# Kernel optimization log

Hardware: AMD Instinct MI355X
Metric: run time of the kernel (lower is better)

## Reference

```python
import jax, jax.numpy as jnp
import numpy as np

B, TMAX, C, H, NCLS = 256, 512, 128, 256, 400


def _lengths():
    rs = np.random.RandomState(0)
    lens = rs.randint(128, TMAX + 1, size=B)
    lens[0] = TMAX  # pin max length so T = TMAX
    return lens


def setup_inputs() -> dict:
    lens = _lengths()
    total = int(lens.sum())
    key = jax.random.key(0)
    ks = jax.random.split(key, 12)
    s_in, s_h = 1.0 / np.sqrt(C), 1.0 / np.sqrt(H)
    return {
        "input_features": jax.random.normal(ks[0], (total, C), jnp.float32),
        "segment_lengths": jnp.asarray(lens, jnp.int32),
        "W_ih": jax.random.normal(ks[1], (4 * H, C), jnp.float32) * s_h,
        "W_hh": jax.random.normal(ks[2], (4 * H, H), jnp.float32) * s_h,
        "b_ih": jax.random.normal(ks[3], (4 * H,), jnp.float32) * s_h,
        "b_hh": jax.random.normal(ks[4], (4 * H,), jnp.float32) * s_h,
        "h0_W1": jax.random.normal(ks[5], (C, C), jnp.float32) * s_in,
        "h0_W2": jax.random.normal(ks[6], (H, C), jnp.float32) * s_in,
        "c0_W1": jax.random.normal(ks[7], (C, C), jnp.float32) * s_in,
        "c0_W2": jax.random.normal(ks[8], (H, C), jnp.float32) * s_in,
        "fc_W": jax.random.normal(ks[9], (NCLS, H), jnp.float32) * s_h,
        "fc_b": jax.random.normal(ks[10], (NCLS,), jnp.float32) * s_h,
    }


def _lstm_step(x, h, c, W_ih, W_hh, b_ih, b_hh):
    # torch.nn.LSTMCell gate order: i, f, g, o
    gates = x @ W_ih.T + b_ih + h @ W_hh.T + b_hh
    i, f, g, o = jnp.split(gates, 4, axis=-1)
    c_new = jax.nn.sigmoid(f) * c + jax.nn.sigmoid(i) * jnp.tanh(g)
    h_new = jax.nn.sigmoid(o) * jnp.tanh(c_new)
    return h_new, c_new


def reference(input_features, segment_lengths, W_ih, W_hh, b_ih, b_hh,
              h0_W1, h0_W2, c0_W1, c0_W2, fc_W, fc_b):
    lens = np.asarray(segment_lengths)            # static ragged structure
    nb = lens.shape[0]
    T = int(lens.max())
    seg_id = np.repeat(np.arange(nb), lens)       # [total]
    offs = np.concatenate([np.arange(l) for l in lens])
    dt = input_features.dtype

    # pad_sequence(batch_first=True): [B, T, C]
    padded = jnp.zeros((nb, T, input_features.shape[1]), dt)
    padded = padded.at[jnp.asarray(seg_id), jnp.asarray(offs)].set(input_features)

    # 'input_means' in the original is actually a per-segment SUM
    sums = jax.ops.segment_sum(input_features, jnp.asarray(seg_id), num_segments=nb)
    h0 = jax.nn.relu(sums @ h0_W1.T) @ h0_W2.T
    c0 = jax.nn.relu(sums @ c0_W1.T) @ c0_W2.T

    def step(carry, x_t):
        h, c = carry
        h, c = _lstm_step(x_t, h, c, W_ih, W_hh, b_ih, b_hh)
        return (h, c), h

    xs = jnp.transpose(padded, (1, 0, 2))         # [T, B, C]
    _, h_outs = jax.lax.scan(step, (h0, c0), xs)  # [T, B, H]

    # Faithful to the original: h_outs is stacked time-first, yet indexed
    # h_outs[i, :segment_len] with i = batch index -> for segment i, mean over
    # the first min(len_i, B) BATCH rows of the hidden state at time t=i.
    lens_j = jnp.asarray(lens)
    mask = (jnp.arange(nb)[None, :] < lens_j[:, None]).astype(dt)   # [B(i), B(b)]
    count = jnp.minimum(lens_j, nb).astype(dt)                       # slice clamps at B
    fc_in = jnp.einsum('ib,ibh->ih', mask, h_outs[:nb]) / count[:, None]

    return fc_in @ fc_W.T + fc_b
```

## Files before the change

### kernel.cpp

```cpp
#include <hip/hip_runtime.h>
#include <hip/hip_bf16.h>
#include <stdint.h>

#define NB    256
#define CIN   128
#define HID   256
#define TST   256
#define NCLS  400

#define GRPS  16
#define MEMB  4
#define BPG   16
#define HPB   64
#define RPB   256
#define HXS   392
#define SPP   17

#define WS_SUMS   0u
#define WS_HEX    131072u
#define WS_C0     655360u
#define WS_TAGS   917504u
#define WS_PP     1048576u

typedef __attribute__((ext_vector_type(8))) short bf16x8;
typedef __attribute__((ext_vector_type(4))) float f32x4;
typedef unsigned long long u64;

__device__ __forceinline__ short f2bf(float f) {
  __hip_bfloat16 h = __float2bfloat16(f);
  return *reinterpret_cast<short*>(&h);
}
__device__ __forceinline__ float sigm(float v) { return 1.0f / (1.0f + __expf(-v)); }
__device__ __forceinline__ float tanh_(float v) {
  v = fminf(fmaxf(v, -15.0f), 15.0f);
  const float e = __expf(2.0f * v);
  return (e - 1.0f) / (e + 1.0f);
}

__global__ void k_segsum(const float* __restrict__ x, const int* __restrict__ lens,
                         float* __restrict__ sums) {
  const int b = blockIdx.x, t = threadIdx.x;
  __shared__ int   s_l[NB];
  __shared__ int   s_red[256];
  __shared__ float s_f[CIN];
  s_l[t] = lens[t];
  __syncthreads();
  int part = 0;
  for (int i = t; i < b; i += 256) part += s_l[i];
  s_red[t] = part; __syncthreads();
  for (int k = 128; k > 0; k >>= 1) { if (t < k) s_red[t] += s_red[t + k]; __syncthreads(); }
  const int off = s_red[0];
  const int len = s_l[b];
  const int c = t & 127, half = t >> 7;
  float a = 0.f;
  for (int r = half; r < len; r += 2) a += x[(size_t)(off + r) * CIN + c];
  if (half) s_f[c] = a;
  __syncthreads();
  if (!half) sums[b * CIN + c] = a + s_f[c];
}

__global__ void k_init(const float* __restrict__ sums,
                       const float* __restrict__ w1h, const float* __restrict__ w2h,
                       const float* __restrict__ w1c, const float* __restrict__ w2c,
                       u64* __restrict__ hexch, float* __restrict__ c0) {
  const int b = blockIdx.x, t = threadIdx.x;
  __shared__ float s_in[CIN], s_h[CIN], s_c[CIN];
  __shared__ __align__(8) short s_hb[HID];
  if (t < CIN) s_in[t] = sums[b * CIN + t];
  __syncthreads();
  {
    const int j = t & 127;
    const float* w = (t < CIN ? w1h : w1c) + j * CIN;
    float a = 0.f;
    #pragma unroll 8
    for (int k = 0; k < CIN; k++) a += s_in[k] * w[k];
    a = fmaxf(a, 0.f);
    if (t < CIN) s_h[j] = a; else s_c[j] = a;
  }
  __syncthreads();
  float ah = 0.f, ac = 0.f;
  const float* wh = w2h + t * CIN;
  const float* wc = w2c + t * CIN;
  #pragma unroll 8
  for (int k = 0; k < CIN; k++) { ah += s_h[k] * wh[k]; ac += s_c[k] * wc[k]; }
  s_hb[t] = f2bf(ah);
  c0[b * HID + t] = ac;
  __syncthreads();
  if (t < HID / 4)
    hexch[(size_t)b * 64 + t] = *(const u64*)&s_hb[t * 4];
}

__launch_bounds__(1024, 1)
__global__ void k_lstm(const float* __restrict__ x, const int* __restrict__ lens,
                       const float* __restrict__ Wih, const float* __restrict__ Whh,
                       const float* __restrict__ bih, const float* __restrict__ bhh,
                       const float* __restrict__ c0,
                       u64* __restrict__ hexch, float* __restrict__ pp,
                       int* __restrict__ tags) {
  const int p    = blockIdx.x;
  const int m    = p >> 4;
  const int grp  = p & 15;
  const int bat0 = grp * BPG;
  const int hid0 = m * HPB;

  const int t   = threadIdx.x;
  const int w   = t >> 6;
  const int kq  = w & 3;
  const int mq  = w >> 2;
  const int l15 = t & 15;
  const int hi  = (t >> 4) & 3;

  const int j2 = t & 63, b2 = t >> 6;
  const int ch = t & 127, bp2 = (t >> 7) * 2;

  __shared__ __align__(16) short s_hxb[BPG * HXS];
  __shared__ float s_part[4 * RPB * SPP];
  __shared__ float s_red[1024];
  __shared__ __align__(8) short s_hvalb[1024];
  __shared__ int   s_lens[NB];
  __shared__ int   s_off[BPG], s_len[BPG];

  if (t < NB) s_lens[t] = lens[t];
  __syncthreads();
  if (t < BPG) {
    int off = 0;
    for (int k = 0; k < bat0 + t; k++) off += s_lens[k];
    s_off[t] = off;
    s_len[t] = s_lens[bat0 + t];
  }
  __syncthreads();

  #define LOADA(AV, MT, KC) do {                                                   \
    const int lr_   = (MT) * 16 + l15;                                             \
    const int grow_ = (lr_ >> 6) * HID + hid0 + (lr_ & 63);                        \
    const int k0_   = kq * 96 + (KC) * 32 + hi * 8;                                \
    const float* src_ = (k0_ < CIN) ? (Wih + (size_t)grow_ * CIN + k0_)            \
                                    : (Whh + (size_t)grow_ * HID + (k0_ - CIN));   \
    const float4 f0_ = *(const float4*)(src_);                                     \
    const float4 f1_ = *(const float4*)(src_ + 4);                                 \
    AV[0]=f2bf(f0_.x); AV[1]=f2bf(f0_.y); AV[2]=f2bf(f0_.z); AV[3]=f2bf(f0_.w);    \
    AV[4]=f2bf(f1_.x); AV[5]=f2bf(f1_.y); AV[6]=f2bf(f1_.z); AV[7]=f2bf(f1_.w);    \
  } while (0)
  bf16x8 a00, a01, a02, a10, a11, a12, a20, a21, a22, a30, a31, a32;
  LOADA(a00, mq*4+0, 0); LOADA(a01, mq*4+0, 1); LOADA(a02, mq*4+0, 2);
  LOADA(a10, mq*4+1, 0); LOADA(a11, mq*4+1, 1); LOADA(a12, mq*4+1, 2);
  LOADA(a20, mq*4+2, 0); LOADA(a21, mq*4+2, 1); LOADA(a22, mq*4+2, 2);
  LOADA(a30, mq*4+3, 0); LOADA(a31, mq*4+3, 1); LOADA(a32, mq*4+3, 2);

  const float bias0 = bih[0*HID + hid0 + j2] + bhh[0*HID + hid0 + j2];
  const float bias1 = bih[1*HID + hid0 + j2] + bhh[1*HID + hid0 + j2];
  const float bias2 = bih[2*HID + hid0 + j2] + bhh[2*HID + hid0 + j2];
  const float bias3 = bih[3*HID + hid0 + j2] + bhh[3*HID + hid0 + j2];

  float c_reg = c0[(size_t)(bat0 + b2) * HID + hid0 + j2];

  float xp0, xp1;
  #define PREFX(S) do { \
    xp0 = ((S) < s_len[bp2+0]) ? x[(size_t)(s_off[bp2+0]+(S))*CIN+ch] : 0.f; \
    xp1 = ((S) < s_len[bp2+1]) ? x[(size_t)(s_off[bp2+1]+(S))*CIN+ch] : 0.f; \
  } while (0)
  #define STAGE(S) do { \
    s_hxb[(bp2+0)*HXS+ch] = f2bf(xp0); \
    s_hxb[(bp2+1)*HXS+ch] = f2bf(xp1); \
    const int b_ = t >> 6, q64_ = t & 63; \
    const int mem_ = q64_ >> 4; \
    if (mem_ == m && (S) > 0) { \
      *(u64*)&s_hxb[b_ * HXS + CIN + q64_ * 4] = \
          *(const u64*)&s_hvalb[b_ * HPB + (q64_ & 15) * 4]; \
    } else { \
      int* tg_ = tags + (((S) & 1) * GRPS + grp) * 16 + mem_ * 4; \
      if (__hip_atomic_load(tg_, __ATOMIC_RELAXED, __HIP_MEMORY_SCOPE_AGENT) < (S)) { \
        while (__hip_atomic_load(tg_, __ATOMIC_RELAXED, __HIP_MEMORY_SCOPE_AGENT) < (S)) \
          __builtin_amdgcn_s_sleep(1); \
      } \
      const u64 v_ = __hip_atomic_load( \
          hexch + ((size_t)((S) & 1) * NB + bat0 + b_) * 64 + q64_, \
          __ATOMIC_RELAXED, __HIP_MEMORY_SCOPE_AGENT); \
      *(u64*)&s_hxb[b_ * HXS + CIN + q64_ * 4] = v_; \
    } \
  } while (0)

  PREFX(0);
  STAGE(0);
  __syncthreads();

  for (int s = 0; s < TST; s++) {
    f32x4 d0 = {0.f,0.f,0.f,0.f}, d1 = {0.f,0.f,0.f,0.f};
    f32x4 d2 = {0.f,0.f,0.f,0.f}, d3 = {0.f,0.f,0.f,0.f};
    {
      const short* hxb = s_hxb + l15 * HXS + kq * 96 + hi * 8;
      bf16x8 bv;
      bv = *(const bf16x8*)(hxb + 0);
      d0 = __builtin_amdgcn_mfma_f32_16x16x32_bf16(a00, bv, d0, 0, 0, 0);
      d1 = __builtin_amdgcn_mfma_f32_16x16x32_bf16(a10, bv, d1, 0, 0, 0);
      d2 = __builtin_amdgcn_mfma_f32_16x16x32_bf16(a20, bv, d2, 0, 0, 0);
      d3 = __builtin_amdgcn_mfma_f32_16x16x32_bf16(a30, bv, d3, 0, 0, 0);
      bv = *(const bf16x8*)(hxb + 32);
      d0 = __builtin_amdgcn_mfma_f32_16x16x32_bf16(a01, bv, d0, 0, 0, 0);
      d1 = __builtin_amdgcn_mfma_f32_16x16x32_bf16(a11, bv, d1, 0, 0, 0);
      d2 = __builtin_amdgcn_mfma_f32_16x16x32_bf16(a21, bv, d2, 0, 0, 0);
      d3 = __builtin_amdgcn_mfma_f32_16x16x32_bf16(a31, bv, d3, 0, 0, 0);
      bv = *(const bf16x8*)(hxb + 64);
      d0 = __builtin_amdgcn_mfma_f32_16x16x32_bf16(a02, bv, d0, 0, 0, 0);
      d1 = __builtin_amdgcn_mfma_f32_16x16x32_bf16(a12, bv, d1, 0, 0, 0);
      d2 = __builtin_amdgcn_mfma_f32_16x16x32_bf16(a22, bv, d2, 0, 0, 0);
      d3 = __builtin_amdgcn_mfma_f32_16x16x32_bf16(a32, bv, d3, 0, 0, 0);
    }
    if (s < TST - 1) PREFX(s + 1);

    {
      float* spc = s_part + (size_t)(kq * RPB + mq * 64 + hi * 4) * SPP + l15;
      spc[(0*16 + 0)*SPP] = d0[0]; spc[(0*16 + 1)*SPP] = d0[1];
      spc[(0*16 + 2)*SPP] = d0[2]; spc[(0*16 + 3)*SPP] = d0[3];
      spc[(1*16 + 0)*SPP] = d1[0]; spc[(1*16 + 1)*SPP] = d1[1];
      spc[(1*16 + 2)*SPP] = d1[2]; spc[(1*16 + 3)*SPP] = d1[3];
      spc[(2*16 + 0)*SPP] = d2[0]; spc[(2*16 + 1)*SPP] = d2[1];
      spc[(2*16 + 2)*SPP] = d2[2]; spc[(2*16 + 3)*SPP] = d2[3];
      spc[(3*16 + 0)*SPP] = d3[0]; spc[(3*16 + 1)*SPP] = d3[1];
      spc[(3*16 + 2)*SPP] = d3[2]; spc[(3*16 + 3)*SPP] = d3[3];
    }
    __syncthreads();

    float g0 = bias0, g1 = bias1, g2 = bias2, g3 = bias3;
    #pragma unroll
    for (int q = 0; q < 4; q++) {
      const float* spq = s_part + (size_t)(q * RPB + j2) * SPP + b2;
      g0 += spq[(0 * 64) * SPP];
      g1 += spq[(1 * 64) * SPP];
      g2 += spq[(2 * 64) * SPP];
      g3 += spq[(3 * 64) * SPP];
    }
    c_reg = fmaf(sigm(g1), c_reg, sigm(g0) * tanh_(g2));
    const float h = sigm(g3) * tanh_(c_reg);

    s_hvalb[b2 * HPB + j2] = f2bf(h);
    s_red[b2 * HPB + j2]   = (bat0 + b2 < s_lens[s]) ? h : 0.f;
    __syncthreads();

    if (t < 256) {
      const int bb = t >> 4, qq = t & 15;
      const u64 v = *(const u64*)&s_hvalb[bb * HPB + qq * 4];
      __hip_atomic_store(
          hexch + ((size_t)((s + 1) & 1) * NB + bat0 + bb) * 64 + (hid0 >> 2) + qq,
          v, __ATOMIC_RELAXED, __HIP_MEMORY_SCOPE_AGENT);
    }
    if (t >= 512 && t < 512 + HPB) {
      const int jl = t - 512;
      float ps = 0.f;
      #pragma unroll
      for (int b = 0; b < BPG; b++) ps += s_red[b * HPB + jl];
      pp[(((size_t)s * GRPS + grp) * MEMB + m) * HPB + jl] = ps;
    }

    if (s == TST - 1) break;

    __syncthreads();

    if (t == 0)
      __hip_atomic_store(tags + (((s + 1) & 1) * GRPS + grp) * 16 + m * 4,
                         s + 1, __ATOMIC_RELAXED, __HIP_MEMORY_SCOPE_AGENT);
    STAGE(s + 1);
    __syncthreads();
  }
}

__global__ void k_out(const float* __restrict__ pp, const int* __restrict__ lens,
                      const float* __restrict__ fcW, const float* __restrict__ fcb,
                      float* __restrict__ out) {
  const int i = blockIdx.x, t = threadIdx.x;
  __shared__ float s_fc[HID];
  const int cnt = min(lens[i], NB);
  const int m = t >> 6, jl = t & 63;
  float a = 0.f;
  const float* base = pp + ((size_t)i * GRPS * MEMB + m) * HPB + jl;
  #pragma unroll 4
  for (int g = 0; g < GRPS; g++) a += base[(size_t)g * MEMB * HPB];
  s_fc[t] = a / (float)cnt;
  __syncthreads();
  for (int n = t; n < NCLS; n += 256) {
    float acc = fcb[n];
    const float4* w4 = (const float4*)(fcW + (size_t)n * HID);
    #pragma unroll 8
    for (int k4 = 0; k4 < HID / 4; k4++) {
      const float4 wv = w4[k4];
      acc = fmaf(s_fc[4*k4+0], wv.x, acc);
      acc = fmaf(s_fc[4*k4+1], wv.y, acc);
      acc = fmaf(s_fc[4*k4+2], wv.z, acc);
      acc = fmaf(s_fc[4*k4+3], wv.w, acc);
    }
    out[(size_t)i * NCLS + n] = acc;
  }
}

extern "C" void kernel_launch(void* const* d_in, const int* in_sizes, int n_in,
                              void* d_out, int out_size, void* d_ws, size_t ws_size,
                              hipStream_t stream) {
  const float* x    = (const float*)d_in[0];
  const int*   lens = (const int*)  d_in[1];
  const float* Wih  = (const float*)d_in[2];
  const float* Whh  = (const float*)d_in[3];
  const float* bih  = (const float*)d_in[4];
  const float* bhh  = (const float*)d_in[5];
  const float* w1h  = (const float*)d_in[6];
  const float* w2h  = (const float*)d_in[7];
  const float* w1c  = (const float*)d_in[8];
  const float* w2c  = (const float*)d_in[9];
  const float* fcW  = (const float*)d_in[10];
  const float* fcb  = (const float*)d_in[11];
  float* out = (float*)d_out;

  char* ws = (char*)d_ws;
  float* sums = (float*)(ws + WS_SUMS);
  u64*   hex  = (u64*)  (ws + WS_HEX);
  float* c0   = (float*)(ws + WS_C0);
  int*   tags = (int*)  (ws + WS_TAGS);
  float* pp   = (float*)(ws + WS_PP);

  hipMemsetAsync(tags, 0, 2 * GRPS * 16 * sizeof(int), stream);
  k_segsum<<<NB, 256, 0, stream>>>(x, lens, sums);
  k_init  <<<NB, 256, 0, stream>>>(sums, w1h, w2h, w1c, w2c, hex, c0);
  k_lstm  <<<GRPS * MEMB, 1024, 0, stream>>>(x, lens, Wih, Whh, bih, bhh, c0, hex, pp, tags);
  k_out   <<<NB, 256, 0, stream>>>(pp, lens, fcW, fcb, out);
}
```

Baseline: 853.5 us.

## Pack step tag with 12-bit quantized hidden state into one exchange word

```diff
diff --git a/kernel.cpp b/kernel.cpp
--- a/kernel.cpp
+++ b/kernel.cpp
@@ -17,10 +17,10 @@
 #define SPP   17
 
 #define WS_SUMS   0u
-#define WS_HEX    131072u
-#define WS_C0     655360u
-#define WS_TAGS   917504u
-#define WS_PP     1048576u
+#define WS_HEX0   131072u
+#define WS_HEX    262144u
+#define WS_C0     524288u
+#define WS_PP     786432u
 
 typedef __attribute__((ext_vector_type(8))) short bf16x8;
 typedef __attribute__((ext_vector_type(4))) float f32x4;
@@ -35,6 +35,15 @@
   v = fminf(fmaxf(v, -15.0f), 15.0f);
   const float e = __expf(2.0f * v);
   return (e - 1.0f) / (e + 1.0f);
+}
+__device__ __forceinline__ int q12(float h) {
+  int q = (int)rintf(h * 2048.f);
+  q = max(-2048, min(2047, q));
+  return q & 0xFFF;
+}
+__device__ __forceinline__ short dq12(int bits) {
+  int q = (bits ^ 0x800) - 0x800;
+  return f2bf((float)q * (1.0f / 2048.f));
 }
 
 __global__ void k_segsum(const float* __restrict__ x, const int* __restrict__ lens,
@@ -62,7 +71,7 @@
 __global__ void k_init(const float* __restrict__ sums,
                        const float* __restrict__ w1h, const float* __restrict__ w2h,
                        const float* __restrict__ w1c, const float* __restrict__ w2c,
-                       u64* __restrict__ hexch, float* __restrict__ c0) {
+                       u64* __restrict__ hex0, float* __restrict__ c0) {
   const int b = blockIdx.x, t = threadIdx.x;
   __shared__ float s_in[CIN], s_h[CIN], s_c[CIN];
   __shared__ __align__(8) short s_hb[HID];
@@ -87,7 +96,7 @@
   c0[b * HID + t] = ac;
   __syncthreads();
   if (t < HID / 4)
-    hexch[(size_t)b * 64 + t] = *(const u64*)&s_hb[t * 4];
+    hex0[(size_t)b * 64 + t] = *(const u64*)&s_hb[t * 4];
 }
 
 __launch_bounds__(1024, 1)
@@ -95,8 +104,8 @@
                        const float* __restrict__ Wih, const float* __restrict__ Whh,
                        const float* __restrict__ bih, const float* __restrict__ bhh,
                        const float* __restrict__ c0,
-                       u64* __restrict__ hexch, float* __restrict__ pp,
-                       int* __restrict__ tags) {
+                       const u64* __restrict__ hex0, u64* __restrict__ hexch,
+                       float* __restrict__ pp) {
   const int p    = blockIdx.x;
   const int m    = p >> 4;
   const int grp  = p & 15;
@@ -159,29 +168,40 @@
     xp0 = ((S) < s_len[bp2+0]) ? x[(size_t)(s_off[bp2+0]+(S))*CIN+ch] : 0.f; \
     xp1 = ((S) < s_len[bp2+1]) ? x[(size_t)(s_off[bp2+1]+(S))*CIN+ch] : 0.f; \
   } while (0)
+
+  #define STAGE0() do { \
+    s_hxb[(bp2+0)*HXS+ch] = f2bf(xp0); \
+    s_hxb[(bp2+1)*HXS+ch] = f2bf(xp1); \
+    const int b_ = t >> 6, q64_ = t & 63; \
+    const u64 v_ = hex0[(size_t)(bat0 + b_) * 64 + q64_]; \
+    *(u64*)&s_hxb[b_ * HXS + CIN + q64_ * 4] = v_; \
+  } while (0)
+
   #define STAGE(S) do { \
     s_hxb[(bp2+0)*HXS+ch] = f2bf(xp0); \
     s_hxb[(bp2+1)*HXS+ch] = f2bf(xp1); \
     const int b_ = t >> 6, q64_ = t & 63; \
     const int mem_ = q64_ >> 4; \
-    if (mem_ == m && (S) > 0) { \
+    if (mem_ == m) { \
       *(u64*)&s_hxb[b_ * HXS + CIN + q64_ * 4] = \
           *(const u64*)&s_hvalb[b_ * HPB + (q64_ & 15) * 4]; \
     } else { \
-      int* tg_ = tags + (((S) & 1) * GRPS + grp) * 16 + mem_ * 4; \
-      if (__hip_atomic_load(tg_, __ATOMIC_RELAXED, __HIP_MEMORY_SCOPE_AGENT) < (S)) { \
-        while (__hip_atomic_load(tg_, __ATOMIC_RELAXED, __HIP_MEMORY_SCOPE_AGENT) < (S)) \
-          __builtin_amdgcn_s_sleep(1); \
+      const u64* src_ = hexch + ((size_t)((S) & 1) * NB + bat0 + b_) * 64 + q64_; \
+      u64 v_ = __hip_atomic_load(src_, __ATOMIC_RELAXED, __HIP_MEMORY_SCOPE_AGENT); \
+      while ((v_ >> 48) != (u64)(S)) { \
+        __builtin_amdgcn_s_sleep(1); \
+        v_ = __hip_atomic_load(src_, __ATOMIC_RELAXED, __HIP_MEMORY_SCOPE_AGENT); \
       } \
-      const u64 v_ = __hip_atomic_load( \
-          hexch + ((size_t)((S) & 1) * NB + bat0 + b_) * 64 + q64_, \
-          __ATOMIC_RELAXED, __HIP_MEMORY_SCOPE_AGENT); \
-      *(u64*)&s_hxb[b_ * HXS + CIN + q64_ * 4] = v_; \
+      short* dst_ = &s_hxb[b_ * HXS + CIN + q64_ * 4]; \
+      dst_[0] = dq12((int)(v_        & 0xFFF)); \
+      dst_[1] = dq12((int)((v_ >> 12) & 0xFFF)); \
+      dst_[2] = dq12((int)((v_ >> 24) & 0xFFF)); \
+      dst_[3] = dq12((int)((v_ >> 36) & 0xFFF)); \
     } \
   } while (0)
 
   PREFX(0);
-  STAGE(0);
+  STAGE0();
   __syncthreads();
 
   for (int s = 0; s < TST; s++) {
@@ -233,17 +253,23 @@
     c_reg = fmaf(sigm(g1), c_reg, sigm(g0) * tanh_(g2));
     const float h = sigm(g3) * tanh_(c_reg);
 
+    {
+      const int q  = q12(h);
+      const int qp = q | (__shfl_xor(q, 1) << 12);
+      const int qo = __shfl_xor(qp, 2);
+      if ((t & 3) == 0) {
+        const u64 v = ((u64)(s + 1) << 48) |
+                      ((u64)(unsigned)(qo & 0xFFFFFF) << 24) |
+                      (u64)(unsigned)(qp & 0xFFFFFF);
+        __hip_atomic_store(
+            hexch + ((size_t)((s + 1) & 1) * NB + bat0 + b2) * 64 + (hid0 >> 2) + (j2 >> 2),
+            v, __ATOMIC_RELAXED, __HIP_MEMORY_SCOPE_AGENT);
+      }
+    }
     s_hvalb[b2 * HPB + j2] = f2bf(h);
     s_red[b2 * HPB + j2]   = (bat0 + b2 < s_lens[s]) ? h : 0.f;
     __syncthreads();
 
-    if (t < 256) {
-      const int bb = t >> 4, qq = t & 15;
-      const u64 v = *(const u64*)&s_hvalb[bb * HPB + qq * 4];
-      __hip_atomic_store(
-          hexch + ((size_t)((s + 1) & 1) * NB + bat0 + bb) * 64 + (hid0 >> 2) + qq,
-          v, __ATOMIC_RELAXED, __HIP_MEMORY_SCOPE_AGENT);
-    }
     if (t >= 512 && t < 512 + HPB) {
       const int jl = t - 512;
       float ps = 0.f;
@@ -254,11 +280,6 @@
 
     if (s == TST - 1) break;
 
-    __syncthreads();
-
-    if (t == 0)
-      __hip_atomic_store(tags + (((s + 1) & 1) * GRPS + grp) * 16 + m * 4,
-                         s + 1, __ATOMIC_RELAXED, __HIP_MEMORY_SCOPE_AGENT);
     STAGE(s + 1);
     __syncthreads();
   }
@@ -311,14 +332,14 @@
 
   char* ws = (char*)d_ws;
   float* sums = (float*)(ws + WS_SUMS);
+  u64*   hex0 = (u64*)  (ws + WS_HEX0);
   u64*   hex  = (u64*)  (ws + WS_HEX);
   float* c0   = (float*)(ws + WS_C0);
-  int*   tags = (int*)  (ws + WS_TAGS);
   float* pp   = (float*)(ws + WS_PP);
 
-  hipMemsetAsync(tags, 0, 2 * GRPS * 16 * sizeof(int), stream);
+  hipMemsetAsync(hex, 0, 2 * NB * 64 * sizeof(u64), stream);
   k_segsum<<<NB, 256, 0, stream>>>(x, lens, sums);
-  k_init  <<<NB, 256, 0, stream>>>(sums, w1h, w2h, w1c, w2c, hex, c0);
-  k_lstm  <<<GRPS * MEMB, 1024, 0, stream>>>(x, lens, Wih, Whh, bih, bhh, c0, hex, pp, tags);
+  k_init  <<<NB, 256, 0, stream>>>(sums, w1h, w2h, w1c, w2c, hex0, c0);
+  k_lstm  <<<GRPS * MEMB, 1024, 0, stream>>>(x, lens, Wih, Whh, bih, bhh, c0, hex0, hex, pp);
   k_out   <<<NB, 256, 0, stream>>>(pp, lens, fcW, fcb, out);
 }
```

Measured after the change: 836.2 us. -2.0%, faster.
